# Optimization experiments

Hardware: AMD Instinct MI355X
Metric: run time of the kernel (lower is better)

The kernel has to match this reference:

```python
import jax, jax.numpy as jnp
import numpy as np

K = 10
A_JAC = 0.5
B_JAC = 0.5
N_NODES = 100000
N_EDGES = 1600000
IN_CH, HID, OUT_CH = 256, 64, 32
NUM_LAYERS = 2


def setup_inputs() -> dict:
    key = jax.random.key(0)
    k1, k2, k3, k4, k5, k6 = jax.random.split(key, 6)
    x = jax.random.normal(k1, (N_NODES, IN_CH), dtype=jnp.float32)
    edge_index = jax.random.randint(k2, (2, N_EDGES), 0, N_NODES, dtype=jnp.int64)
    W1 = jax.random.normal(k3, (IN_CH, HID), dtype=jnp.float32) / np.sqrt(IN_CH)
    b1 = jnp.zeros((HID,), dtype=jnp.float32)
    coeffs = jnp.ones((NUM_LAYERS, K + 1), dtype=jnp.float32) / (K + 1)
    W2 = jax.random.normal(k4, (HID, OUT_CH), dtype=jnp.float32) / np.sqrt(HID)
    b2 = jnp.zeros((OUT_CH,), dtype=jnp.float32)
    return {"x": x, "edge_index": edge_index, "W1": W1, "b1": b1,
            "coeffs": coeffs, "W2": W2, "b2": b2}


def _build_norm(edge_index, num_nodes):
    # add self loops (as PyG add_self_loops does)
    loops = jnp.arange(num_nodes, dtype=edge_index.dtype)
    row = jnp.concatenate([edge_index[0], loops])
    col = jnp.concatenate([edge_index[1], loops])
    deg = jax.ops.segment_sum(jnp.ones_like(col, dtype=jnp.float32), col,
                              num_segments=num_nodes)
    dinv = jnp.where(deg > 0, deg ** -0.5, 0.0)
    norm = dinv[row] * dinv[col]  # [E + N]
    return row, col, norm


def _propagate(h, row, col, norm, num_nodes):
    # out[i] = sum_{e: col[e]=i} norm[e] * h[row[e]]
    return jax.ops.segment_sum(norm[:, None] * h[row], col, num_segments=num_nodes)


def _jacobi_conv(h, row, col, norm, c, num_nodes):
    a, b = A_JAC, B_JAC
    Tx0 = h
    out = c[0] * Tx0
    Tx1 = _propagate(h, row, col, norm, num_nodes)
    out = out + c[1] * Tx1
    for k in range(2, K + 1):
        n = k - 1
        A_n = (2 * n + a + b + 1) * (2 * n + a + b + 2) / (2 * (n + 1) * (n + a + b + 1))
        B_n = (a ** 2 - b ** 2) * (2 * n + a + b + 1) / (2 * (n + 1) * (n + a + b + 1) * (2 * n + a + b))
        C_n = (n + a) * (n + b) * (2 * n + a + b + 2) / ((n + 1) * (n + a + b + 1) * (2 * n + a + b))
        Tx2 = A_n * _propagate(Tx1, row, col, norm, num_nodes) + B_n * Tx1 - C_n * Tx0
        out = out + c[k] * Tx2
        Tx0, Tx1 = Tx1, Tx2
    return out


def reference(x, edge_index, W1, b1, coeffs, W2, b2):
    num_nodes = x.shape[0]
    row, col, norm = _build_norm(edge_index, num_nodes)
    h = jax.nn.relu(x @ W1 + b1)
    for l in range(NUM_LAYERS):
        h = jax.nn.relu(_jacobi_conv(h, row, col, norm, coeffs[l], num_nodes))
    return h @ W2 + b2
```

## Files before the change

kernel.cpp:

```cpp
#include <hip/hip_runtime.h>
#include <hip/hip_fp16.h>

#define NN 100000
#define NE 1600000
#define KORD 10
#define HID 64

#define NBUK ((NN + 255) / 256)
#define BCAP 8192
#define EPB  (NE / 256)
#define CSR_CAP (NE + 8 * NN)

typedef _Float16 half8v __attribute__((ext_vector_type(8)));
typedef _Float16 half4v __attribute__((ext_vector_type(4)));
typedef float float4v __attribute__((ext_vector_type(4)));
typedef unsigned uint4v __attribute__((ext_vector_type(4)));
typedef int int4v __attribute__((ext_vector_type(4)));

__device__ __forceinline__ float2 up2(unsigned u) {
    __half2 hh = *(__half2*)&u;
    return __half22float2(hh);
}
__device__ __forceinline__ unsigned pk2(float a, float b) {
    __half2 hh = __floats2half2_rn(a, b);
    return *(unsigned*)&hh;
}

__global__ __launch_bounds__(512) void k_zero(int* __restrict__ gcnt,
                                              int* __restrict__ dhist,
                                              int* __restrict__ palloc) {
    int t = threadIdx.x;
    if (t < NBUK) gcnt[t] = 0;
    if (t < 64) dhist[t] = 0;
    if (t == 511) *palloc = 0;
}

__global__ __launch_bounds__(1024) void k_binA(const int* __restrict__ ei,
                                               int* __restrict__ gcnt,
                                               unsigned* __restrict__ staged) {
    __shared__ int lh[NBUK];
    __shared__ int lcur[NBUK];
    int t = threadIdx.x;
    int ebeg = blockIdx.x * EPB;
    int eend = min(ebeg + EPB, NE);
    for (int i = t; i < NBUK; i += 1024) lh[i] = 0;
    __syncthreads();
    for (int e = ebeg + t; e < eend; e += 1024)
        atomicAdd(&lh[ei[NE + e] >> 8], 1);
    __syncthreads();
    for (int i = t; i < NBUK; i += 1024)
        lcur[i] = lh[i] ? atomicAdd(&gcnt[i], lh[i]) : 0;
    __syncthreads();
    for (int e = ebeg + t; e < eend; e += 1024) {
        int r = ei[e], c = ei[NE + e];
        int bkt = c >> 8;
        int slot = atomicAdd(&lcur[bkt], 1);
        if (slot < BCAP)
            staged[(size_t)bkt * BCAP + slot] = ((unsigned)(c & 255) << 24) | (unsigned)r;
    }
}

__global__ __launch_bounds__(512) void k_binB(const unsigned* __restrict__ staged,
                                              const int* __restrict__ gcnt,
                                              int* __restrict__ palloc,
                                              int* __restrict__ cnt,
                                              float* __restrict__ dinv,
                                              int* __restrict__ csr,
                                              int2* __restrict__ seg) {
    __shared__ unsigned lrec[BCAP];
    __shared__ int lcnt[256], lcur[256], ltmp[256];
    __shared__ int lbase;
    int b = blockIdx.x, t = threadIdx.x;
    int count = min(gcnt[b], BCAP);
    if (t < 256) lcnt[t] = 0;
    __syncthreads();
    for (int i = t; i < count; i += 512) {
        unsigned rec = staged[(size_t)b * BCAP + i];
        lrec[i] = rec;
        atomicAdd(&lcnt[rec >> 24], 1);
    }
    __syncthreads();
    int v = 0, plen = 0;
    if (t < 256) { v = lcnt[t]; plen = (v + 7) & ~7; ltmp[t] = plen; }
    __syncthreads();
    int x = plen;
    for (int off = 1; off < 256; off <<= 1) {
        int y = (t < 256 && t >= off) ? ltmp[t - off] : 0;
        __syncthreads();
        if (t < 256) { x += y; ltmp[t] = x; }
        __syncthreads();
    }
    if (t == 255) lbase = atomicAdd(palloc, x);
    __syncthreads();
    int start = 0;
    if (t < 256) {
        start = lbase + x - plen;
        lcur[t] = start;
        int node = b * 256 + t;
        if (node < NN) {
            cnt[node] = v;
            dinv[node] = rsqrtf((float)(v + 1));
            seg[node] = make_int2(start, plen >> 3);
            for (int i = v; i < plen; ++i) csr[start + i] = NN;
        }
    }
    __syncthreads();
    for (int i = t; i < count; i += 512) {
        unsigned rec = lrec[i];
        int pos = atomicAdd(&lcur[rec >> 24], 1);
        csr[pos] = (int)(rec & 0xFFFFFFu);
    }
}

__global__ __launch_bounds__(256) void k_dhist(const int* __restrict__ cnt,
                                               int* __restrict__ dhist) {
    __shared__ int lh[64];
    int t = threadIdx.x;
    if (t < 64) lh[t] = 0;
    __syncthreads();
    int i = blockIdx.x * 256 + t;
    if (i < NN) atomicAdd(&lh[min(cnt[i], 63)], 1);
    __syncthreads();
    if (t < 64 && lh[t]) atomicAdd(&dhist[t], lh[t]);
}

__global__ void k_dscan(int* __restrict__ dhist) {
    __shared__ int tmp[64];
    int t = threadIdx.x;
    int v = dhist[t];
    tmp[t] = v;
    __syncthreads();
    int x = v;
    for (int off = 1; off < 64; off <<= 1) {
        int y = (t >= off) ? tmp[t - off] : 0;
        __syncthreads();
        x += y;
        tmp[t] = x;
        __syncthreads();
    }
    dhist[t] = x - v;
}

__global__ __launch_bounds__(256) void k_dperm(const int* __restrict__ cnt,
                                               int* __restrict__ dhist,
                                               int* __restrict__ perm) {
    __shared__ int lh[64], lb[64];
    int t = threadIdx.x;
    if (t < 64) lh[t] = 0;
    __syncthreads();
    int i = blockIdx.x * 256 + t;
    int b = 0, my = 0;
    if (i < NN) { b = min(cnt[i], 63); my = atomicAdd(&lh[b], 1); }
    __syncthreads();
    if (t < 64) lb[t] = lh[t] ? atomicAdd(&dhist[t], lh[t]) : 0;
    __syncthreads();
    if (i < NN) perm[lb[b] + my] = i;
}

__global__ __launch_bounds__(256) void k_zrow(__half* __restrict__ a, __half* __restrict__ b,
                                              __half* __restrict__ c, __half* __restrict__ d) {
    int t = threadIdx.x;
    __half z = __float2half(0.f);
    size_t base = (size_t)NN * HID;
    if (t < 64)       a[base + t] = z;
    else if (t < 128) b[base + (t - 64)] = z;
    else if (t < 192) c[base + (t - 128)] = z;
    else              d[base + (t - 192)] = z;
}

__global__ __launch_bounds__(256) void k_prepw1(const float* __restrict__ W1,
                                                _Float16* __restrict__ W1T) {
    int f = blockIdx.x * 256 + threadIdx.x;
    int n = f >> 8, k = f & 255;
    W1T[f] = (_Float16)W1[k * 64 + n];
}

#define G1K 128
#define G1S 136
__global__ __launch_bounds__(256) void k_gemm1(const float* __restrict__ x,
                                               const _Float16* __restrict__ W1T,
                                               const float* __restrict__ b1,
                                               const float* __restrict__ dinv,
                                               __half* __restrict__ h) {
    __shared__ _Float16 A_lds[64 * G1S];
    __shared__ _Float16 B_lds[64 * G1S];
    int t = threadIdx.x;
    int wave = t >> 6, lane = t & 63;
    int quad = lane >> 4, m16 = lane & 15;
    int row0 = blockIdx.x * 64;

    float4v acc[4];
#pragma unroll
    for (int n4 = 0; n4 < 4; ++n4) acc[n4] = (float4v){0.f, 0.f, 0.f, 0.f};

    for (int c = 0; c < 2; ++c) {
        int k0 = c * G1K;
#pragma unroll
        for (int i = 0; i < 8; ++i) {
            int f = i * 256 + t;
            int r = f >> 5, c4 = f & 31;
            int grow = row0 + r;
            float4 v = (grow < NN) ? *(const float4*)&x[(size_t)grow * 256 + k0 + c4 * 4]
                                   : make_float4(0.f, 0.f, 0.f, 0.f);
            half4v hv = {(_Float16)v.x, (_Float16)v.y, (_Float16)v.z, (_Float16)v.w};
            *(half4v*)&A_lds[r * G1S + c4 * 4] = hv;
        }
#pragma unroll
        for (int i = 0; i < 4; ++i) {
            int f = i * 256 + t;
            int n = f >> 4, k8 = f & 15;
            *(half8v*)&B_lds[n * G1S + k8 * 8] =
                *(const half8v*)&W1T[n * 256 + k0 + k8 * 8];
        }
        __syncthreads();

#pragma unroll
        for (int s = 0; s < 4; ++s) {
            half8v af = *(const half8v*)&A_lds[(wave * 16 + m16) * G1S + s * 32 + quad * 8];
#pragma unroll
            for (int n4 = 0; n4 < 4; ++n4) {
                half8v bf = *(const half8v*)&B_lds[(n4 * 16 + m16) * G1S + s * 32 + quad * 8];
                acc[n4] = __builtin_amdgcn_mfma_f32_16x16x32_f16(af, bf, acc[n4], 0, 0, 0);
            }
        }
        __syncthreads();
    }

    float bv[4];
#pragma unroll
    for (int n4 = 0; n4 < 4; ++n4) bv[n4] = b1[n4 * 16 + m16];
#pragma unroll
    for (int r = 0; r < 4; ++r) {
        int grow = row0 + wave * 16 + quad * 4 + r;
        if (grow >= NN) continue;
        float dv = dinv[grow];
#pragma unroll
        for (int n4 = 0; n4 < 4; ++n4) {
            float v = dv * fmaxf(acc[n4][r] + bv[n4], 0.f);
            h[(size_t)grow * 64 + n4 * 16 + m16] = __float2half(v);
        }
    }
}

#define ACCV(u) { p01 += up2((u).x); p23 += up2((u).y); p45 += up2((u).z); p67 += up2((u).w); }

__global__ __launch_bounds__(256) void k_prop(const int2* __restrict__ seg,
                                              const int* __restrict__ csr,
                                              const int* __restrict__ perm,
                                              const __half* __restrict__ src,
                                              const __half* __restrict__ t0,
                                              const float* __restrict__ dinv,
                                              __half* __restrict__ dst,
                                              __half* __restrict__ acc,
                                              __half* __restrict__ hout,
                                              float An, float Bn, float Cn,
                                              const float* __restrict__ coeffs,
                                              int cbase, int kidx, int init,
                                              int finalize, int unscale) {
    int slot = ((blockIdx.x * 256 + threadIdx.x) >> 6) * 8 + ((threadIdx.x & 63) >> 3);
    int ch8 = (threadIdx.x & 7) * 8;
    bool valid = slot < NN;
    int node = valid ? perm[slot] : 0;
    int2 sg = valid ? seg[node] : make_int2(0, 0);
    const int4v* cp = (const int4v*)(csr + sg.x);
    int iters = sg.y;

    size_t idx = (size_t)node * HID + ch8;
    float dv = dinv[node];
    float ck = coeffs[cbase + kidx];
    float c0 = coeffs[cbase];
    uint4v sr = *(const uint4v*)&src[idx];
    uint4v tr = *(const uint4v*)&t0[idx];
    uint4v ar = {0u, 0u, 0u, 0u};
    if (!init) ar = *(const uint4v*)&acc[idx];

    float2 p01 = {0.f, 0.f}, p23 = {0.f, 0.f}, p45 = {0.f, 0.f}, p67 = {0.f, 0.f};

    int4v ia, ib;
    if (iters > 0) { ia = cp[0]; ib = cp[1]; }
    for (int it = 0; it < iters; ++it) {
        uint4v u0 = *(const uint4v*)&src[(size_t)ia.x * HID + ch8];
        uint4v u1 = *(const uint4v*)&src[(size_t)ia.y * HID + ch8];
        uint4v u2 = *(const uint4v*)&src[(size_t)ia.z * HID + ch8];
        uint4v u3 = *(const uint4v*)&src[(size_t)ia.w * HID + ch8];
        uint4v u4 = *(const uint4v*)&src[(size_t)ib.x * HID + ch8];
        uint4v u5 = *(const uint4v*)&src[(size_t)ib.y * HID + ch8];
        uint4v u6 = *(const uint4v*)&src[(size_t)ib.z * HID + ch8];
        uint4v u7 = *(const uint4v*)&src[(size_t)ib.w * HID + ch8];
        if (it + 1 < iters) {
            ia = cp[it * 2 + 2];
            ib = cp[it * 2 + 3];
        }
        ACCV(u0); ACCV(u1); ACCV(u2); ACCV(u3);
        ACCV(u4); ACCV(u5); ACCV(u6); ACCV(u7);
    }

    if (!valid) return;
    float dv2 = dv * dv;
    float p[8] = {p01.x, p01.y, p23.x, p23.y, p45.x, p45.y, p67.x, p67.y};

    float2 s01 = up2(sr.x), s23 = up2(sr.y), s45 = up2(sr.z), s67 = up2(sr.w);
    float sv[8] = {s01.x, s01.y, s23.x, s23.y, s45.x, s45.y, s67.x, s67.y};

    float2 t01 = up2(tr.x), t23 = up2(tr.y), t45 = up2(tr.z), t67 = up2(tr.w);
    float tv[8] = {t01.x, t01.y, t23.x, t23.y, t45.x, t45.y, t67.x, t67.y};

    float v[8];
#pragma unroll
    for (int i = 0; i < 8; ++i)
        v[i] = An * dv2 * (p[i] + sv[i]) + Bn * sv[i] - Cn * tv[i];

    if (!finalize) {
        uint4v o;
        o.x = pk2(v[0], v[1]); o.y = pk2(v[2], v[3]);
        o.z = pk2(v[4], v[5]); o.w = pk2(v[6], v[7]);
        *(uint4v*)&dst[idx] = o;
    }

    float av[8];
    if (init) {
#pragma unroll
        for (int i = 0; i < 8; ++i) av[i] = c0 * sv[i];
    } else {
        float2 a01 = up2(ar.x), a23 = up2(ar.y), a45 = up2(ar.z), a67 = up2(ar.w);
        av[0] = a01.x; av[1] = a01.y; av[2] = a23.x; av[3] = a23.y;
        av[4] = a45.x; av[5] = a45.y; av[6] = a67.x; av[7] = a67.y;
    }
#pragma unroll
    for (int i = 0; i < 8; ++i) av[i] += ck * v[i];

    uint4v o;
    if (finalize) {
        float s = unscale ? (1.0f / dv) : 1.0f;
        o.x = pk2(s * fmaxf(av[0], 0.f), s * fmaxf(av[1], 0.f));
        o.y = pk2(s * fmaxf(av[2], 0.f), s * fmaxf(av[3], 0.f));
        o.z = pk2(s * fmaxf(av[4], 0.f), s * fmaxf(av[5], 0.f));
        o.w = pk2(s * fmaxf(av[6], 0.f), s * fmaxf(av[7], 0.f));
        *(uint4v*)&hout[idx] = o;
    } else {
        o.x = pk2(av[0], av[1]); o.y = pk2(av[2], av[3]);
        o.z = pk2(av[4], av[5]); o.w = pk2(av[6], av[7]);
        *(uint4v*)&acc[idx] = o;
    }
}

__global__ __launch_bounds__(256) void k_gemm2(const __half* __restrict__ h,
                                               const float* __restrict__ W2,
                                               const float* __restrict__ b2,
                                               float* __restrict__ out) {
    __shared__ float W2s[64 * 32];
    __shared__ float b2s[32];
    int t = threadIdx.x;
    for (int i = t * 4; i < 64 * 32; i += 256 * 4)
        *(float4*)&W2s[i] = *(const float4*)&W2[i];
    if (t < 32) b2s[t] = b2[t];
    __syncthreads();

    int gid = blockIdx.x * 256 + t;
    int row = gid >> 3;
    int c4 = (t & 7) * 4;
    if (row >= NN) return;
    const __half* hr = h + (size_t)row * 64;
    float4 acc = *(const float4*)&b2s[c4];
#pragma unroll
    for (int k8 = 0; k8 < 8; ++k8) {
        uint4 raw = *(const uint4*)&hr[k8 * 8];
        float2 a01 = up2(raw.x), a23 = up2(raw.y), a45 = up2(raw.z), a67 = up2(raw.w);
        float a[8] = {a01.x, a01.y, a23.x, a23.y, a45.x, a45.y, a67.x, a67.y};
#pragma unroll
        for (int j = 0; j < 8; ++j) {
            float4 w = *(const float4*)&W2s[(k8 * 8 + j) * 32 + c4];
            acc.x += a[j] * w.x;
            acc.y += a[j] * w.y;
            acc.z += a[j] * w.z;
            acc.w += a[j] * w.w;
        }
    }
    *(float4*)&out[(size_t)row * 32 + c4] = acc;
}

extern "C" void kernel_launch(void* const* d_in, const int* in_sizes, int n_in,
                              void* d_out, int out_size, void* d_ws, size_t ws_size,
                              hipStream_t stream) {
    const float* x      = (const float*)d_in[0];
    const int*   ei     = (const int*)d_in[1];
    const float* W1     = (const float*)d_in[2];
    const float* b1     = (const float*)d_in[3];
    const float* coeffs = (const float*)d_in[4];
    const float* W2     = (const float*)d_in[5];
    const float* b2     = (const float*)d_in[6];
    float* out = (float*)d_out;

    char* ws = (char*)d_ws;
    size_t off = 0;
    auto alloc = [&](size_t bytes) { void* p = ws + off; off += (bytes + 255) & ~(size_t)255; return p; };
    int*      cnt    = (int*)alloc(NN * 4);
    float*    dinv   = (float*)alloc(NN * 4);
    int*      csr    = (int*)alloc((size_t)CSR_CAP * 4);
    int2*     seg    = (int2*)alloc((size_t)NN * 8);
    int*      dhist  = (int*)alloc(64 * 4);
    int*      perm   = (int*)alloc(NN * 4);
    int*      gcnt   = (int*)alloc(NBUK * 4);
    int*      palloc = (int*)alloc(4);
    unsigned* staged = (unsigned*)alloc((size_t)NBUK * BCAP * 4);
    _Float16* W1T    = (_Float16*)alloc(256 * 64 * 2);
    __half*   h16    = (__half*)alloc((size_t)(NN + 1) * HID * 2);
    __half*   bufA   = (__half*)alloc((size_t)(NN + 1) * HID * 2);
    __half*   bufB   = (__half*)alloc((size_t)(NN + 1) * HID * 2);
    __half*   bufC   = (__half*)alloc((size_t)(NN + 1) * HID * 2);
    __half*   accb   = (__half*)alloc((size_t)NN * HID * 2);

    const int BN = (NN + 255) / 256;
    const int BP = (NN + 31) / 32;

    k_zero<<<1, 512, 0, stream>>>(gcnt, dhist, palloc);
    k_binA<<<256, 1024, 0, stream>>>(ei, gcnt, staged);
    k_binB<<<NBUK, 512, 0, stream>>>(staged, gcnt, palloc, cnt, dinv, csr, seg);

    k_dhist<<<BN, 256, 0, stream>>>(cnt, dhist);
    k_dscan<<<1, 64, 0, stream>>>(dhist);
    k_dperm<<<BN, 256, 0, stream>>>(cnt, dhist, perm);
    k_zrow<<<1, 256, 0, stream>>>(h16, bufA, bufB, bufC);

    k_prepw1<<<64, 256, 0, stream>>>(W1, W1T);
    k_gemm1<<<(NN + 63) / 64, 256, 0, stream>>>(x, W1T, b1, dinv, h16);

    __half* rot[4] = {h16, bufA, bufB, bufC};

    for (int l = 0; l < 2; ++l) {
        int cbase = l * (KORD + 1);
        k_prop<<<BP, 256, 0, stream>>>(seg, csr, perm, rot[0], rot[0], dinv,
                                       rot[1], accb, h16, 1.0f, 0.0f, 0.0f,
                                       coeffs, cbase, 1, 1, 0, 0);
        for (int k = 2; k <= KORD; ++k) {
            __half* dst = rot[k & 3];
            const __half* s1 = rot[(k - 1) & 3];
            const __half* s0 = rot[(k - 2) & 3];
            double n = k - 1, a = 0.5, b = 0.5;
            double An = (2*n + a + b + 1) * (2*n + a + b + 2) / (2 * (n + 1) * (n + a + b + 1));
            double Bn = (a*a - b*b) * (2*n + a + b + 1) / (2 * (n + 1) * (n + a + b + 1) * (2*n + a + b));
            double Cn = (n + a) * (n + b) * (2*n + a + b + 2) / ((n + 1) * (n + a + b + 1) * (2*n + a + b));
            k_prop<<<BP, 256, 0, stream>>>(seg, csr, perm, s1, s0, dinv,
                                           dst, accb, h16, (float)An, (float)Bn, (float)Cn,
                                           coeffs, cbase, k, 0,
                                           (k == KORD) ? 1 : 0, l);
        }
    }

    k_gemm2<<<(NN * 8 + 255) / 256, 256, 0, stream>>>(h16, W2, b2, out);
}
```

Baseline: 976.4 us.

## Sort CSR neighbors by source range and process two node groups per block

Within each destination node's CSR segment, edges are now bucketed into four source-index ranges, so neighbor gathers walk source rows in a more ordered way and may get better cache locality. The propagation kernel also launches half as many blocks, with each thread handling two slots spaced PBLK blocks apart. This amortizes the coefficient loads and block scheduling. The cost is extra shared-memory counters in binning and a longer serial path per thread, which may reduce latency hiding.

```diff
diff --git a/kernel.cpp b/kernel.cpp
--- a/kernel.cpp
+++ b/kernel.cpp
@@ -10,6 +10,9 @@
 #define BCAP 8192
 #define EPB  (NE / 256)
 #define CSR_CAP (NE + 8 * NN)
+
+#define PBLK ((NN + 63) / 64)
+#define NSLOT1 (PBLK * 32)
 
 typedef _Float16 half8v __attribute__((ext_vector_type(8)));
 typedef _Float16 half4v __attribute__((ext_vector_type(4)));
@@ -68,20 +71,30 @@
                                               int* __restrict__ csr,
                                               int2* __restrict__ seg) {
     __shared__ unsigned lrec[BCAP];
-    __shared__ int lcnt[256], lcur[256], ltmp[256];
+    __shared__ int lcnt2[1024];
+    __shared__ int lcur2[1024];
+    __shared__ int ltmp[256];
     __shared__ int lbase;
     int b = blockIdx.x, t = threadIdx.x;
     int count = min(gcnt[b], BCAP);
-    if (t < 256) lcnt[t] = 0;
+    for (int i = t; i < 1024; i += 512) lcnt2[i] = 0;
     __syncthreads();
     for (int i = t; i < count; i += 512) {
         unsigned rec = staged[(size_t)b * BCAP + i];
         lrec[i] = rec;
-        atomicAdd(&lcnt[rec >> 24], 1);
-    }
-    __syncthreads();
-    int v = 0, plen = 0;
-    if (t < 256) { v = lcnt[t]; plen = (v + 7) & ~7; ltmp[t] = plen; }
+        unsigned src = rec & 0xFFFFFFu;
+        int sl = (int)(src / 25000u);
+        atomicAdd(&lcnt2[((rec >> 24) << 2) | sl], 1);
+    }
+    __syncthreads();
+    int v = 0, plen = 0, c0 = 0, c1 = 0, c2 = 0, c3 = 0;
+    if (t < 256) {
+        c0 = lcnt2[t * 4];     c1 = lcnt2[t * 4 + 1];
+        c2 = lcnt2[t * 4 + 2]; c3 = lcnt2[t * 4 + 3];
+        v = c0 + c1 + c2 + c3;
+        plen = (v + 7) & ~7;
+        ltmp[t] = plen;
+    }
     __syncthreads();
     int x = plen;
     for (int off = 1; off < 256; off <<= 1) {
@@ -92,10 +105,12 @@
     }
     if (t == 255) lbase = atomicAdd(palloc, x);
     __syncthreads();
-    int start = 0;
     if (t < 256) {
-        start = lbase + x - plen;
-        lcur[t] = start;
+        int start = lbase + x - plen;
+        lcur2[t * 4]     = start;
+        lcur2[t * 4 + 1] = start + c0;
+        lcur2[t * 4 + 2] = start + c0 + c1;
+        lcur2[t * 4 + 3] = start + c0 + c1 + c2;
         int node = b * 256 + t;
         if (node < NN) {
             cnt[node] = v;
@@ -107,8 +122,10 @@
     __syncthreads();
     for (int i = t; i < count; i += 512) {
         unsigned rec = lrec[i];
-        int pos = atomicAdd(&lcur[rec >> 24], 1);
-        csr[pos] = (int)(rec & 0xFFFFFFu);
+        unsigned src = rec & 0xFFFFFFu;
+        int sl = (int)(src / 25000u);
+        int pos = atomicAdd(&lcur2[((rec >> 24) << 2) | sl], 1);
+        csr[pos] = (int)src;
     }
 }
 
@@ -257,90 +274,97 @@
                                               const float* __restrict__ coeffs,
                                               int cbase, int kidx, int init,
                                               int finalize, int unscale) {
-    int slot = ((blockIdx.x * 256 + threadIdx.x) >> 6) * 8 + ((threadIdx.x & 63) >> 3);
-    int ch8 = (threadIdx.x & 7) * 8;
-    bool valid = slot < NN;
-    int node = valid ? perm[slot] : 0;
-    int2 sg = valid ? seg[node] : make_int2(0, 0);
-    const int4v* cp = (const int4v*)(csr + sg.x);
-    int iters = sg.y;
-
-    size_t idx = (size_t)node * HID + ch8;
-    float dv = dinv[node];
+    int t = threadIdx.x;
+    int lg = (t >> 6) * 8 + ((t & 63) >> 3);
+    int ch8 = (t & 7) * 8;
     float ck = coeffs[cbase + kidx];
     float c0 = coeffs[cbase];
-    uint4v sr = *(const uint4v*)&src[idx];
-    uint4v tr = *(const uint4v*)&t0[idx];
-    uint4v ar = {0u, 0u, 0u, 0u};
-    if (!init) ar = *(const uint4v*)&acc[idx];
-
-    float2 p01 = {0.f, 0.f}, p23 = {0.f, 0.f}, p45 = {0.f, 0.f}, p67 = {0.f, 0.f};
-
-    int4v ia, ib;
-    if (iters > 0) { ia = cp[0]; ib = cp[1]; }
-    for (int it = 0; it < iters; ++it) {
-        uint4v u0 = *(const uint4v*)&src[(size_t)ia.x * HID + ch8];
-        uint4v u1 = *(const uint4v*)&src[(size_t)ia.y * HID + ch8];
-        uint4v u2 = *(const uint4v*)&src[(size_t)ia.z * HID + ch8];
-        uint4v u3 = *(const uint4v*)&src[(size_t)ia.w * HID + ch8];
-        uint4v u4 = *(const uint4v*)&src[(size_t)ib.x * HID + ch8];
-        uint4v u5 = *(const uint4v*)&src[(size_t)ib.y * HID + ch8];
-        uint4v u6 = *(const uint4v*)&src[(size_t)ib.z * HID + ch8];
-        uint4v u7 = *(const uint4v*)&src[(size_t)ib.w * HID + ch8];
-        if (it + 1 < iters) {
-            ia = cp[it * 2 + 2];
-            ib = cp[it * 2 + 3];
-        }
-        ACCV(u0); ACCV(u1); ACCV(u2); ACCV(u3);
-        ACCV(u4); ACCV(u5); ACCV(u6); ACCV(u7);
-    }
-
-    if (!valid) return;
-    float dv2 = dv * dv;
-    float p[8] = {p01.x, p01.y, p23.x, p23.y, p45.x, p45.y, p67.x, p67.y};
-
-    float2 s01 = up2(sr.x), s23 = up2(sr.y), s45 = up2(sr.z), s67 = up2(sr.w);
-    float sv[8] = {s01.x, s01.y, s23.x, s23.y, s45.x, s45.y, s67.x, s67.y};
-
-    float2 t01 = up2(tr.x), t23 = up2(tr.y), t45 = up2(tr.z), t67 = up2(tr.w);
-    float tv[8] = {t01.x, t01.y, t23.x, t23.y, t45.x, t45.y, t67.x, t67.y};
-
-    float v[8];
-#pragma unroll
-    for (int i = 0; i < 8; ++i)
-        v[i] = An * dv2 * (p[i] + sv[i]) + Bn * sv[i] - Cn * tv[i];
-
-    if (!finalize) {
-        uint4v o;
-        o.x = pk2(v[0], v[1]); o.y = pk2(v[2], v[3]);
-        o.z = pk2(v[4], v[5]); o.w = pk2(v[6], v[7]);
-        *(uint4v*)&dst[idx] = o;
-    }
-
-    float av[8];
-    if (init) {
-#pragma unroll
-        for (int i = 0; i < 8; ++i) av[i] = c0 * sv[i];
-    } else {
-        float2 a01 = up2(ar.x), a23 = up2(ar.y), a45 = up2(ar.z), a67 = up2(ar.w);
-        av[0] = a01.x; av[1] = a01.y; av[2] = a23.x; av[3] = a23.y;
-        av[4] = a45.x; av[5] = a45.y; av[6] = a67.x; av[7] = a67.y;
-    }
-#pragma unroll
-    for (int i = 0; i < 8; ++i) av[i] += ck * v[i];
-
-    uint4v o;
-    if (finalize) {
-        float s = unscale ? (1.0f / dv) : 1.0f;
-        o.x = pk2(s * fmaxf(av[0], 0.f), s * fmaxf(av[1], 0.f));
-        o.y = pk2(s * fmaxf(av[2], 0.f), s * fmaxf(av[3], 0.f));
-        o.z = pk2(s * fmaxf(av[4], 0.f), s * fmaxf(av[5], 0.f));
-        o.w = pk2(s * fmaxf(av[6], 0.f), s * fmaxf(av[7], 0.f));
-        *(uint4v*)&hout[idx] = o;
-    } else {
-        o.x = pk2(av[0], av[1]); o.y = pk2(av[2], av[3]);
-        o.z = pk2(av[4], av[5]); o.w = pk2(av[6], av[7]);
-        *(uint4v*)&acc[idx] = o;
+
+#pragma unroll
+    for (int g = 0; g < 2; ++g) {
+        int slot = (blockIdx.x + g * PBLK) * 32 + lg;
+        bool valid = slot < NN;
+        int node = valid ? perm[slot] : 0;
+        int2 sg = valid ? seg[node] : make_int2(0, 0);
+        const int4v* cp = (const int4v*)(csr + sg.x);
+        int iters = sg.y;
+
+        size_t idx = (size_t)node * HID + ch8;
+        float dv = dinv[node];
+        uint4v sr = *(const uint4v*)&src[idx];
+        uint4v tr = *(const uint4v*)&t0[idx];
+        uint4v ar = {0u, 0u, 0u, 0u};
+        if (!init) ar = *(const uint4v*)&acc[idx];
+
+        float2 p01 = {0.f, 0.f}, p23 = {0.f, 0.f}, p45 = {0.f, 0.f}, p67 = {0.f, 0.f};
+
+        int4v ia = {0, 0, 0, 0}, ib = {0, 0, 0, 0};
+        if (iters > 0) { ia = cp[0]; ib = cp[1]; }
+        for (int it = 0; it < iters; ++it) {
+            uint4v u0 = *(const uint4v*)&src[(size_t)ia.x * HID + ch8];
+            uint4v u1 = *(const uint4v*)&src[(size_t)ia.y * HID + ch8];
+            uint4v u2 = *(const uint4v*)&src[(size_t)ia.z * HID + ch8];
+            uint4v u3 = *(const uint4v*)&src[(size_t)ia.w * HID + ch8];
+            uint4v u4 = *(const uint4v*)&src[(size_t)ib.x * HID + ch8];
+            uint4v u5 = *(const uint4v*)&src[(size_t)ib.y * HID + ch8];
+            uint4v u6 = *(const uint4v*)&src[(size_t)ib.z * HID + ch8];
+            uint4v u7 = *(const uint4v*)&src[(size_t)ib.w * HID + ch8];
+            if (it + 1 < iters) {
+                ia = cp[it * 2 + 2];
+                ib = cp[it * 2 + 3];
+            }
+            ACCV(u0); ACCV(u1); ACCV(u2); ACCV(u3);
+            ACCV(u4); ACCV(u5); ACCV(u6); ACCV(u7);
+        }
+
+        if (valid) {
+            float dv2 = dv * dv;
+            float p[8] = {p01.x, p01.y, p23.x, p23.y, p45.x, p45.y, p67.x, p67.y};
+
+            float2 s01 = up2(sr.x), s23 = up2(sr.y), s45 = up2(sr.z), s67 = up2(sr.w);
+            float sv[8] = {s01.x, s01.y, s23.x, s23.y, s45.x, s45.y, s67.x, s67.y};
+
+            float2 t01 = up2(tr.x), t23 = up2(tr.y), t45 = up2(tr.z), t67 = up2(tr.w);
+            float tv[8] = {t01.x, t01.y, t23.x, t23.y, t45.x, t45.y, t67.x, t67.y};
+
+            float v[8];
+#pragma unroll
+            for (int i = 0; i < 8; ++i)
+                v[i] = An * dv2 * (p[i] + sv[i]) + Bn * sv[i] - Cn * tv[i];
+
+            if (!finalize) {
+                uint4v o;
+                o.x = pk2(v[0], v[1]); o.y = pk2(v[2], v[3]);
+                o.z = pk2(v[4], v[5]); o.w = pk2(v[6], v[7]);
+                *(uint4v*)&dst[idx] = o;
+            }
+
+            float av[8];
+            if (init) {
+#pragma unroll
+                for (int i = 0; i < 8; ++i) av[i] = c0 * sv[i];
+            } else {
+                float2 a01 = up2(ar.x), a23 = up2(ar.y), a45 = up2(ar.z), a67 = up2(ar.w);
+                av[0] = a01.x; av[1] = a01.y; av[2] = a23.x; av[3] = a23.y;
+                av[4] = a45.x; av[5] = a45.y; av[6] = a67.x; av[7] = a67.y;
+            }
+#pragma unroll
+            for (int i = 0; i < 8; ++i) av[i] += ck * v[i];
+
+            uint4v o;
+            if (finalize) {
+                float s = unscale ? (1.0f / dv) : 1.0f;
+                o.x = pk2(s * fmaxf(av[0], 0.f), s * fmaxf(av[1], 0.f));
+                o.y = pk2(s * fmaxf(av[2], 0.f), s * fmaxf(av[3], 0.f));
+                o.z = pk2(s * fmaxf(av[4], 0.f), s * fmaxf(av[5], 0.f));
+                o.w = pk2(s * fmaxf(av[6], 0.f), s * fmaxf(av[7], 0.f));
+                *(uint4v*)&hout[idx] = o;
+            } else {
+                o.x = pk2(av[0], av[1]); o.y = pk2(av[2], av[3]);
+                o.z = pk2(av[4], av[5]); o.w = pk2(av[6], av[7]);
+                *(uint4v*)&acc[idx] = o;
+            }
+        }
     }
 }
 
@@ -411,7 +435,6 @@
     __half*   accb   = (__half*)alloc((size_t)NN * HID * 2);
 
     const int BN = (NN + 255) / 256;
-    const int BP = (NN + 31) / 32;
 
     k_zero<<<1, 512, 0, stream>>>(gcnt, dhist, palloc);
     k_binA<<<256, 1024, 0, stream>>>(ei, gcnt, staged);
@@ -429,9 +452,9 @@
 
     for (int l = 0; l < 2; ++l) {
         int cbase = l * (KORD + 1);
-        k_prop<<<BP, 256, 0, stream>>>(seg, csr, perm, rot[0], rot[0], dinv,
-                                       rot[1], accb, h16, 1.0f, 0.0f, 0.0f,
-                                       coeffs, cbase, 1, 1, 0, 0);
+        k_prop<<<PBLK, 256, 0, stream>>>(seg, csr, perm, rot[0], rot[0], dinv,
+                                         rot[1], accb, h16, 1.0f, 0.0f, 0.0f,
+                                         coeffs, cbase, 1, 1, 0, 0);
         for (int k = 2; k <= KORD; ++k) {
             __half* dst = rot[k & 3];
             const __half* s1 = rot[(k - 1) & 3];
@@ -440,10 +463,10 @@
             double An = (2*n + a + b + 1) * (2*n + a + b + 2) / (2 * (n + 1) * (n + a + b + 1));
             double Bn = (a*a - b*b) * (2*n + a + b + 1) / (2 * (n + 1) * (n + a + b + 1) * (2*n + a + b));
             double Cn = (n + a) * (n + b) * (2*n + a + b + 2) / ((n + 1) * (n + a + b + 1) * (2*n + a + b));
-            k_prop<<<BP, 256, 0, stream>>>(seg, csr, perm, s1, s0, dinv,
-                                           dst, accb, h16, (float)An, (float)Bn, (float)Cn,
-                                           coeffs, cbase, k, 0,
-                                           (k == KORD) ? 1 : 0, l);
+            k_prop<<<PBLK, 256, 0, stream>>>(seg, csr, perm, s1, s0, dinv,
+                                             dst, accb, h16, (float)An, (float)Bn, (float)Cn,
+                                             coeffs, cbase, k, 0,
+                                             (k == KORD) ? 1 : 0, l);
         }
     }
 
```

After: 993.9 us. Within noise of the previous version (+1.8%).
